# Optimization experiments

Measured on AMD Instinct MI355X. Metric: run time of the kernel, lower is better.

Reference implementation:

```python
import jax, jax.numpy as jnp
import numpy as np

N = 8192
E = 262144
H = 64


def setup_inputs() -> dict:
    key = jax.random.key(0)
    ks = jax.random.split(key, 9)
    edge_index = jax.random.randint(ks[0], (2, E), 0, N, dtype=jnp.int64)
    edge_attr = jax.random.uniform(ks[1], (E,), dtype=jnp.float32)
    node_features = jax.random.normal(ks[2], (N, N), dtype=jnp.float32)
    # GCNConv weights (glorot-ish scale) and biases
    W1 = jax.random.normal(ks[3], (N, H), dtype=jnp.float32) / np.sqrt(N)
    b1 = jnp.zeros((H,), dtype=jnp.float32)
    W2 = jax.random.normal(ks[4], (H, H), dtype=jnp.float32) / np.sqrt(H)
    b2 = jnp.zeros((H,), dtype=jnp.float32)
    fcW = jax.random.normal(ks[5], (H, N), dtype=jnp.float32) / np.sqrt(H)
    fcb = jnp.zeros((N,), dtype=jnp.float32)
    return {"edge_index": edge_index, "edge_attr": edge_attr,
            "node_features": node_features,
            "W1": W1, "b1": b1, "W2": W2, "b2": b2,
            "fcW": fcW, "fcb": fcb}


def _gcn_conv(x, W, b, src, dst, ew, n_nodes):
    # PyG GCNConv with edge weights: x' = D^{-1/2} (A + I) D^{-1/2} (x W) + b
    # src/dst/ew already include self-loops (weight 1.0).
    x = x @ W                                        # [N, out]
    deg = jax.ops.segment_sum(ew, dst, num_segments=n_nodes)  # in-degree w/ loops
    dinv = jax.lax.rsqrt(deg)                        # deg >= 1 due to self loops
    norm = dinv[src] * ew * dinv[dst]                # [E+N]
    out = jax.ops.segment_sum(x[src] * norm[:, None], dst, num_segments=n_nodes)
    return out + b


def reference(edge_index, edge_attr, node_features, W1, b1, W2, b2, fcW, fcb):
    n_nodes = node_features.shape[0]
    loops = jnp.arange(n_nodes, dtype=edge_index.dtype)
    src = jnp.concatenate([edge_index[0], loops])
    dst = jnp.concatenate([edge_index[1], loops])
    ew = jnp.concatenate([edge_attr, jnp.ones((n_nodes,), edge_attr.dtype)])
    x = jax.nn.relu(_gcn_conv(node_features, W1, b1, src, dst, ew, n_nodes))
    x = jax.nn.relu(_gcn_conv(x, W2, b2, src, dst, ew, n_nodes))
    x = x @ fcW + fcb
    return jax.nn.softmax(x, axis=-1)
```

## Files before the change

kernel.cpp:

```cpp
#include <hip/hip_runtime.h>


#define NN 8192
#define NE 262144
#define HD 64
#define KCH 1024
#define NKC 8

typedef float f32x4 __attribute__((ext_vector_type(4)));
typedef short v8s   __attribute__((ext_vector_type(8)));
typedef unsigned short ushort_t;

__device__ __forceinline__ unsigned short bf16_rne(float f){
  union { float f; unsigned u; } v; v.f = f;
  unsigned r = v.u + 0x7fffu + ((v.u >> 16) & 1u);
  return (unsigned short)(r >> 16);
}
__device__ __forceinline__ float bf16_f32(unsigned short h){
  union { unsigned u; float f; } v; v.u = ((unsigned)h) << 16;
  return v.f;
}
__device__ __forceinline__ f32x4 mfma16(v8s a, v8s b, f32x4 c){
  return __builtin_amdgcn_mfma_f32_16x16x32_bf16(a, b, c, 0, 0, 0);
}

__global__ void k_prep0(const float* __restrict__ W1, const float* __restrict__ fcW,
                        ushort_t* w1hi, ushort_t* w1lo, ushort_t* fcwp,
                        float* deg, int* cnt, int* wcnt, float* S){
  int idx = blockIdx.x*blockDim.x + threadIdx.x;
  if (idx < NN){ deg[idx]=1.0f; cnt[idx]=0; wcnt[idx]=0; S[idx]=0.0f; }
  {
    int kk = idx & 31, c = (idx>>5)&15, nt = (idx>>9)&3, kb = idx>>11;
    int k = kb*32 + kk, col = nt*16 + c;
    float w = W1[(size_t)k*HD + col];
    unsigned short hi = bf16_rne(w);
    w1hi[idx] = hi;
    w1lo[idx] = bf16_rne(w - bf16_f32(hi));
  }
  {
    int kk = idx & 31, c = (idx>>5)&15, cblk = (idx>>9)&511, kb = idx>>18;
    int k = kb*32 + kk, col = cblk*16 + c;
    fcwp[idx] = bf16_rne(fcW[(size_t)k*NN + col]);
  }
}

__global__ void k_deg_cnt(const int* ei, const float* ew, float* deg, int* cnt){
  int e = blockIdx.x*blockDim.x + threadIdx.x;
  if (e < NE){
    int d = ei[NE + e];
    atomicAdd(&deg[d], ew[e]);
    atomicAdd(&cnt[d], 1);
  }
}

__global__ void k_scan(const int* cnt, const float* deg, int* rowptr, float* dinv){
  __shared__ int part[256];
  int t = threadIdx.x;
  int loc[32]; int s = 0;
  #pragma unroll
  for (int j=0;j<32;++j){ loc[j] = cnt[t*32+j]; s += loc[j]; }
  part[t] = s; __syncthreads();
  for (int off=1; off<256; off<<=1){
    int v = (t >= off) ? part[t-off] : 0;
    __syncthreads();
    part[t] += v;
    __syncthreads();
  }
  int run = part[t] - s;
  #pragma unroll
  for (int j=0;j<32;++j){ rowptr[t*32+j] = run; run += loc[j]; }
  if (t == 255) rowptr[NN] = run;
  #pragma unroll
  for (int j=0;j<32;++j) dinv[t*32+j] = 1.0f / sqrtf(deg[t*32+j]);
}

__global__ void k_fill(const int* ei, const float* ew, const float* dinv,
                       const int* rowptr, int* wcnt, int* csr_src, float* csr_nrm){
  int e = blockIdx.x*blockDim.x + threadIdx.x;
  if (e < NE){
    int s = ei[e], d = ei[NE+e];
    int slot = rowptr[d] + atomicAdd(&wcnt[d], 1);
    csr_src[slot] = s;
    csr_nrm[slot] = dinv[s] * ew[e] * dinv[d];
  }
}

__global__ __launch_bounds__(256) void k_gemm1(const float* __restrict__ X,
                                               const ushort_t* __restrict__ w1hi,
                                               const ushort_t* __restrict__ w1lo,
                                               float* __restrict__ xw1p){
  int lane = threadIdx.x & 63, w = threadIdx.x >> 6;
  int r = lane & 15, seg = lane >> 4;
  int row = blockIdx.x*64 + w*16 + r;
  int kb0 = blockIdx.y * KCH;
  const float* xr = X + (size_t)row * NN + kb0 + seg*8;

  f32x4 z = {0.f,0.f,0.f,0.f};
  f32x4 acc[4] = {z,z,z,z};

  f32x4 p0 = *(const f32x4*)(xr);
  f32x4 p1 = *(const f32x4*)(xr + 4);

  for (int it = 0; it < KCH/32; ++it){
    f32x4 c0 = p0, c1 = p1;
    if (it < KCH/32 - 1){
      p0 = *(const f32x4*)(xr + (it+1)*32);
      p1 = *(const f32x4*)(xr + (it+1)*32 + 4);
    }
    v8s ah, al;
    #pragma unroll
    for (int j=0;j<4;++j){
      float f = c0[j]; unsigned short h = bf16_rne(f);
      ah[j] = (short)h; al[j] = (short)bf16_rne(f - bf16_f32(h));
      f = c1[j]; h = bf16_rne(f);
      ah[4+j] = (short)h; al[4+j] = (short)bf16_rne(f - bf16_f32(h));
    }
    int kbb = (kb0 >> 5) + it;
    #pragma unroll
    for (int nt=0; nt<4; ++nt){
      size_t boff = ((size_t)(kbb*4 + nt)*16 + r)*32 + seg*8;
      v8s bh = *(const v8s*)(w1hi + boff);
      v8s bl = *(const v8s*)(w1lo + boff);
      acc[nt] = mfma16(ah, bh, acc[nt]);
      acc[nt] = mfma16(ah, bl, acc[nt]);
      acc[nt] = mfma16(al, bh, acc[nt]);
    }
  }

  float* o = xw1p + (size_t)blockIdx.y*(NN*HD) + (size_t)(blockIdx.x*64 + w*16)*HD;
  #pragma unroll
  for (int nt=0; nt<4; ++nt)
    #pragma unroll
    for (int j=0;j<4;++j)
      o[(4*seg + j)*HD + nt*16 + r] = acc[nt][j];
}

__global__ __launch_bounds__(256) void k_red(const float* __restrict__ xw1p,
                                             float* __restrict__ xw1){
  int i = blockIdx.x*blockDim.x + threadIdx.x;
  f32x4 s = {0.f,0.f,0.f,0.f};
  #pragma unroll
  for (int c=0;c<NKC;++c){
    f32x4 v = *(const f32x4*)(xw1p + (size_t)c*NN*HD + (size_t)i*4);
    s[0]+=v[0]; s[1]+=v[1]; s[2]+=v[2]; s[3]+=v[3];
  }
  *(f32x4*)(xw1 + (size_t)i*4) = s;
}

__global__ __launch_bounds__(256) void k_agg1c(const float* __restrict__ xin,
                                               const float* __restrict__ b1,
                                               const float* __restrict__ W2,
                                               const float* __restrict__ dinv,
                                               const int* __restrict__ rowptr,
                                               const int* __restrict__ csr_src,
                                               const float* __restrict__ csr_nrm,
                                               float* __restrict__ x2w){
  __shared__ float W2s[64*64];
  __shared__ float rows[4][64];
  int lane = threadIdx.x & 63, w = threadIdx.x >> 6;
  for (int o = threadIdx.x; o < 64*64; o += 256) W2s[o] = W2[o];
  __syncthreads();

  int i = blockIdx.x*4 + w;
  float di = dinv[i];
  float acc = di*di * xin[(size_t)i*HD + lane];
  int e = rowptr[i], e1 = rowptr[i+1];
  for (; e + 1 < e1; e += 2){
    int s0 = csr_src[e], s1 = csr_src[e+1];
    float n0 = csr_nrm[e], n1 = csr_nrm[e+1];
    acc += n0 * xin[(size_t)s0*HD + lane];
    acc += n1 * xin[(size_t)s1*HD + lane];
  }
  if (e < e1) acc += csr_nrm[e] * xin[(size_t)csr_src[e]*HD + lane];
  float v = acc + b1[lane];
  rows[w][lane] = v > 0.f ? v : 0.f;
  __syncthreads();

  float acc2 = 0.f;
  #pragma unroll
  for (int k=0;k<64;++k) acc2 += rows[w][k] * W2s[k*64 + lane];
  x2w[(size_t)i*HD + lane] = acc2;
}

__global__ __launch_bounds__(256) void k_agg2(const float* __restrict__ xin,
                                              const float* __restrict__ b2,
                                              const float* __restrict__ dinv,
                                              const int* __restrict__ rowptr,
                                              const int* __restrict__ csr_src,
                                              const float* __restrict__ csr_nrm,
                                              ushort_t* __restrict__ x2b){
  int lane = threadIdx.x & 63, w = threadIdx.x >> 6;
  int i = blockIdx.x*4 + w;
  float di = dinv[i];
  float acc = di*di * xin[(size_t)i*HD + lane];
  int e = rowptr[i], e1 = rowptr[i+1];
  for (; e + 1 < e1; e += 2){
    int s0 = csr_src[e], s1 = csr_src[e+1];
    float n0 = csr_nrm[e], n1 = csr_nrm[e+1];
    acc += n0 * xin[(size_t)s0*HD + lane];
    acc += n1 * xin[(size_t)s1*HD + lane];
  }
  if (e < e1) acc += csr_nrm[e] * xin[(size_t)csr_src[e]*HD + lane];
  float v = acc + b2[lane];
  v = v > 0.f ? v : 0.f;
  x2b[(size_t)i*HD + lane] = bf16_rne(v);
}

__global__ __launch_bounds__(256) void k_rowsum(const ushort_t* __restrict__ x2b,
                                                const ushort_t* __restrict__ fcwp,
                                                const float* __restrict__ fcb,
                                                float* __restrict__ S){
  int lane = threadIdx.x & 63, w = threadIdx.x >> 6;
  int r = lane & 15, seg = lane >> 4;
  int row0 = blockIdx.x*128 + w*32;
  const ushort_t* xb = x2b + (size_t)(row0 + r)*HD + seg*8;
  v8s x00 = *(const v8s*)(xb);
  v8s x01 = *(const v8s*)(xb + 32);
  v8s x10 = *(const v8s*)(xb + 16*HD);
  v8s x11 = *(const v8s*)(xb + 16*HD + 32);
  float rp0 = 0.f, rp1 = 0.f;
  for (int cb=0; cb<4; ++cb){
    int colbase = blockIdx.y*256 + cb*64;
    f32x4 z = {0.f,0.f,0.f,0.f};
    f32x4 acc0[4] = {z,z,z,z}, acc1[4] = {z,z,z,z};
    #pragma unroll
    for (int nt=0; nt<4; ++nt){
      int cblk = (colbase >> 4) + nt;
      v8s bA = *(const v8s*)(fcwp + ((size_t)cblk*16 + r)*32 + seg*8);
      v8s bB = *(const v8s*)(fcwp + ((size_t)(512 + cblk)*16 + r)*32 + seg*8);
      acc0[nt] = mfma16(bA, x00, acc0[nt]);
      acc0[nt] = mfma16(bB, x01, acc0[nt]);
      acc1[nt] = mfma16(bA, x10, acc1[nt]);
      acc1[nt] = mfma16(bB, x11, acc1[nt]);
    }
    #pragma unroll
    for (int nt=0; nt<4; ++nt){
      int col = colbase + nt*16 + seg*4;
      f32x4 fb = *(const f32x4*)(fcb + col);
      #pragma unroll
      for (int j=0;j<4;++j){
        rp0 += __expf(acc0[nt][j] + fb[j]);
        rp1 += __expf(acc1[nt][j] + fb[j]);
      }
    }
  }
  rp0 += __shfl_xor(rp0, 16); rp0 += __shfl_xor(rp0, 32);
  rp1 += __shfl_xor(rp1, 16); rp1 += __shfl_xor(rp1, 32);
  if (lane < 16){
    atomicAdd(&S[row0 + lane],      rp0);
    atomicAdd(&S[row0 + 16 + lane], rp1);
  }
}

__global__ __launch_bounds__(256) void k_passB(const ushort_t* __restrict__ x2b,
                                               const ushort_t* __restrict__ fcwp,
                                               const float* __restrict__ fcb,
                                               const float* __restrict__ S,
                                               float* __restrict__ out){
  int lane = threadIdx.x & 63, w = threadIdx.x >> 6;
  int r = lane & 15, seg = lane >> 4;
  int row0 = blockIdx.x*128 + w*32;
  const ushort_t* xb = x2b + (size_t)(row0 + r)*HD + seg*8;
  v8s x00 = *(const v8s*)(xb);
  v8s x01 = *(const v8s*)(xb + 32);
  v8s x10 = *(const v8s*)(xb + 16*HD);
  v8s x11 = *(const v8s*)(xb + 16*HD + 32);
  float si0 = 1.0f / S[row0 + r];
  float si1 = 1.0f / S[row0 + 16 + r];
  float* o0 = out + (size_t)(row0 + r)*NN;
  float* o1 = out + (size_t)(row0 + 16 + r)*NN;
  for (int cb=0; cb<4; ++cb){
    int colbase = blockIdx.y*256 + cb*64;
    f32x4 z = {0.f,0.f,0.f,0.f};
    f32x4 acc0[4] = {z,z,z,z}, acc1[4] = {z,z,z,z};
    #pragma unroll
    for (int nt=0; nt<4; ++nt){
      int cblk = (colbase >> 4) + nt;
      v8s bA = *(const v8s*)(fcwp + ((size_t)cblk*16 + r)*32 + seg*8);
      v8s bB = *(const v8s*)(fcwp + ((size_t)(512 + cblk)*16 + r)*32 + seg*8);
      acc0[nt] = mfma16(bA, x00, acc0[nt]);
      acc0[nt] = mfma16(bB, x01, acc0[nt]);
      acc1[nt] = mfma16(bA, x10, acc1[nt]);
      acc1[nt] = mfma16(bB, x11, acc1[nt]);
    }
    #pragma unroll
    for (int nt=0; nt<4; ++nt){
      int col = colbase + nt*16 + seg*4;
      f32x4 fb = *(const f32x4*)(fcb + col);
      f32x4 v0, v1;
      #pragma unroll
      for (int j=0;j<4;++j){
        v0[j] = __expf(acc0[nt][j] + fb[j]) * si0;
        v1[j] = __expf(acc1[nt][j] + fb[j]) * si1;
      }
      *(f32x4*)(o0 + col) = v0;
      *(f32x4*)(o1 + col) = v1;
    }
  }
}

extern "C" void kernel_launch(void* const* d_in, const int* in_sizes, int n_in,
                              void* d_out, int out_size, void* d_ws, size_t ws_size,
                              hipStream_t stream){
  (void)in_sizes; (void)n_in; (void)out_size; (void)ws_size;
  const int*   ei  = (const int*)  d_in[0];
  const float* ew  = (const float*)d_in[1];
  const float* X   = (const float*)d_in[2];
  const float* W1  = (const float*)d_in[3];
  const float* b1  = (const float*)d_in[4];
  const float* W2  = (const float*)d_in[5];
  const float* b2  = (const float*)d_in[6];
  const float* fcW = (const float*)d_in[7];
  const float* fcb = (const float*)d_in[8];
  float* out = (float*)d_out;
  char*  ws  = (char*)d_ws;

  float*    deg     = (float*)   (ws + 0);
  float*    dinv    = (float*)   (ws + 32768);
  int*      cnt     = (int*)     (ws + 65536);
  int*      wcnt    = (int*)     (ws + 98304);
  int*      rowptr  = (int*)     (ws + 131072);
  int*      csr_src = (int*)     (ws + 167936);
  float*    csr_nrm = (float*)   (ws + 1216512);
  ushort_t* w1hi    = (ushort_t*)(ws + 2265088);
  ushort_t* w1lo    = (ushort_t*)(ws + 3313664);
  ushort_t* fcwp    = (ushort_t*)(ws + 4362240);
  float*    xw1p    = (float*)   (ws + 5410816);
  float*    xw1     = (float*)   (ws + 22188032);
  float*    x2w     = (float*)   (ws + 24285184);
  ushort_t* x2b     = (ushort_t*)(ws + 26382336);
  float*    S       = (float*)   (ws + 27430912);

  k_prep0   <<<2048, 256, 0, stream>>>(W1, fcW, w1hi, w1lo, fcwp, deg, cnt, wcnt, S);
  k_deg_cnt <<<1024, 256, 0, stream>>>(ei, ew, deg, cnt);
  k_scan    <<<1,    256, 0, stream>>>(cnt, deg, rowptr, dinv);
  k_fill    <<<1024, 256, 0, stream>>>(ei, ew, dinv, rowptr, wcnt, csr_src, csr_nrm);
  k_gemm1   <<<dim3(128, NKC), 256, 0, stream>>>(X, w1hi, w1lo, xw1p);
  k_red     <<<512,  256, 0, stream>>>(xw1p, xw1);
  k_agg1c   <<<2048, 256, 0, stream>>>(xw1, b1, W2, dinv, rowptr, csr_src, csr_nrm, x2w);
  k_agg2    <<<2048, 256, 0, stream>>>(x2w, b2, dinv, rowptr, csr_src, csr_nrm, x2b);
  k_rowsum  <<<dim3(64,32), 256, 0, stream>>>(x2b, fcwp, fcb, S);
  k_passB   <<<dim3(64,32), 256, 0, stream>>>(x2b, fcwp, fcb, S, out);
}
```

Baseline: 320.8 us.

## Cast X to bf16 once and stage gemm1 tiles through swizzled LDS

Adds a pre-pass that converts the 8192x8192 fp32 feature matrix to bf16 in the output buffer. The first GEMM then reads bf16 tiles into double-buffered, XOR-swizzled shared memory using direct global-to-LDS loads. The split-bf16 hi/lo three-MFMA scheme becomes a single bf16 MFMA, cutting matrix work and per-thread conversion. In exchange it adds a full extra read and write pass over X and loses precision in the first layer's product.

```diff
diff --git a/kernel.cpp b/kernel.cpp
--- a/kernel.cpp
+++ b/kernel.cpp
@@ -6,6 +6,7 @@
 #define HD 64
 #define KCH 1024
 #define NKC 8
+#define NTS (KCH/64)
 
 typedef float f32x4 __attribute__((ext_vector_type(4)));
 typedef short v8s   __attribute__((ext_vector_type(8)));
@@ -23,9 +24,28 @@
 __device__ __forceinline__ f32x4 mfma16(v8s a, v8s b, f32x4 c){
   return __builtin_amdgcn_mfma_f32_16x16x32_bf16(a, b, c, 0, 0, 0);
 }
+__device__ __forceinline__ void gload16(const void* g, void* l){
+  __builtin_amdgcn_global_load_lds(
+      (const __attribute__((address_space(1))) unsigned int*)g,
+      (__attribute__((address_space(3))) unsigned int*)l, 16, 0, 0);
+}
+
+__global__ __launch_bounds__(256) void k_xcast(const float* __restrict__ X,
+                                               ushort_t* __restrict__ xb){
+  size_t i = ((size_t)blockIdx.x*256 + threadIdx.x)*8;
+  f32x4 a = *(const f32x4*)(X + i);
+  f32x4 b = *(const f32x4*)(X + i + 4);
+  v8s o;
+  #pragma unroll
+  for (int j=0;j<4;++j){
+    o[j]   = (short)bf16_rne(a[j]);
+    o[4+j] = (short)bf16_rne(b[j]);
+  }
+  *(v8s*)(xb + i) = o;
+}
 
 __global__ void k_prep0(const float* __restrict__ W1, const float* __restrict__ fcW,
-                        ushort_t* w1hi, ushort_t* w1lo, ushort_t* fcwp,
+                        ushort_t* w1hi, ushort_t* fcwp,
                         float* deg, int* cnt, int* wcnt, float* S){
   int idx = blockIdx.x*blockDim.x + threadIdx.x;
   if (idx < NN){ deg[idx]=1.0f; cnt[idx]=0; wcnt[idx]=0; S[idx]=0.0f; }
@@ -33,9 +53,9 @@
     int kk = idx & 31, c = (idx>>5)&15, nt = (idx>>9)&3, kb = idx>>11;
     int k = kb*32 + kk, col = nt*16 + c;
     float w = W1[(size_t)k*HD + col];
-    unsigned short hi = bf16_rne(w);
-    w1hi[idx] = hi;
-    w1lo[idx] = bf16_rne(w - bf16_f32(hi));
+    int chunk = idx >> 3, e = idx & 7;
+    int sidx = ((chunk ^ (c & 7)) << 3) | e;
+    w1hi[sidx] = bf16_rne(w);
   }
   {
     int kk = idx & 31, c = (idx>>5)&15, cblk = (idx>>9)&511, kb = idx>>18;
@@ -85,49 +105,72 @@
   }
 }
 
-__global__ __launch_bounds__(256) void k_gemm1(const float* __restrict__ X,
-                                               const ushort_t* __restrict__ w1hi,
-                                               const ushort_t* __restrict__ w1lo,
-                                               float* __restrict__ xw1p){
+__global__ __launch_bounds__(256, 4) void k_gemm1(const ushort_t* __restrict__ Xb,
+                                                  const ushort_t* __restrict__ w1hi,
+                                                  float* __restrict__ xw1p){
+  __shared__ __align__(16) char sA[2][8192];
+  __shared__ __align__(16) char sB[2][8192];
   int lane = threadIdx.x & 63, w = threadIdx.x >> 6;
   int r = lane & 15, seg = lane >> 4;
-  int row = blockIdx.x*64 + w*16 + r;
-  int kb0 = blockIdx.y * KCH;
-  const float* xr = X + (size_t)row * NN + kb0 + seg*8;
+  int c8 = lane & 7, r8 = lane >> 3;
+  int row0 = blockIdx.x*64, kb0 = blockIdx.y*KCH;
+
+  const char* Xc  = (const char*)Xb;
+  const char* w1c = (const char*)w1hi;
+  size_t asrc[2];
+  #pragma unroll
+  for (int i=0;i<2;++i){
+    int rl = w*16 + i*8 + r8;
+    asrc[i] = (size_t)(row0 + rl)*(NN*2) + (size_t)kb0*2 + (size_t)((c8 ^ r8)*16);
+  }
+
+  int aoff[2];
+  #pragma unroll
+  for (int ks=0; ks<2; ++ks)
+    aoff[ks] = (w*16 + r)*128 + (((ks*4 + seg) ^ (r & 7)) << 4);
+  int bc[4];
+  #pragma unroll
+  for (int nt=0; nt<4; ++nt)
+    bc[nt] = ((nt*64 + r*4 + seg) ^ (r & 7)) << 4;
 
   f32x4 z = {0.f,0.f,0.f,0.f};
   f32x4 acc[4] = {z,z,z,z};
 
-  f32x4 p0 = *(const f32x4*)(xr);
-  f32x4 p1 = *(const f32x4*)(xr + 4);
-
-  for (int it = 0; it < KCH/32; ++it){
-    f32x4 c0 = p0, c1 = p1;
-    if (it < KCH/32 - 1){
-      p0 = *(const f32x4*)(xr + (it+1)*32);
-      p1 = *(const f32x4*)(xr + (it+1)*32 + 4);
-    }
-    v8s ah, al;
-    #pragma unroll
-    for (int j=0;j<4;++j){
-      float f = c0[j]; unsigned short h = bf16_rne(f);
-      ah[j] = (short)h; al[j] = (short)bf16_rne(f - bf16_f32(h));
-      f = c1[j]; h = bf16_rne(f);
-      ah[4+j] = (short)h; al[4+j] = (short)bf16_rne(f - bf16_f32(h));
-    }
-    int kbb = (kb0 >> 5) + it;
-    #pragma unroll
-    for (int nt=0; nt<4; ++nt){
-      size_t boff = ((size_t)(kbb*4 + nt)*16 + r)*32 + seg*8;
-      v8s bh = *(const v8s*)(w1hi + boff);
-      v8s bl = *(const v8s*)(w1lo + boff);
-      acc[nt] = mfma16(ah, bh, acc[nt]);
-      acc[nt] = mfma16(ah, bl, acc[nt]);
-      acc[nt] = mfma16(al, bh, acc[nt]);
-    }
-  }
-
-  float* o = xw1p + (size_t)blockIdx.y*(NN*HD) + (size_t)(blockIdx.x*64 + w*16)*HD;
+  auto STAGE = [&](int t, int b){
+    char* aD = (char*)sA[b] + w*2048;
+    gload16(Xc + asrc[0] + (size_t)t*128, aD);
+    gload16(Xc + asrc[1] + (size_t)t*128, aD + 1024);
+    size_t sBo = ((size_t)(kb0 >> 5) + 2*t)*4096 + w*1024 + lane*16;
+    gload16(w1c + sBo,        (char*)sB[b] + w*1024);
+    gload16(w1c + sBo + 4096, (char*)sB[b] + 4096 + w*1024);
+  };
+
+  STAGE(0, 0);
+
+  for (int t = 0; t < NTS; ++t){
+    int cur = t & 1;
+    if (t + 1 < NTS){
+      STAGE(t+1, cur^1);
+      asm volatile("s_waitcnt vmcnt(4)" ::: "memory");
+    } else {
+      asm volatile("s_waitcnt vmcnt(0)" ::: "memory");
+    }
+    __builtin_amdgcn_s_barrier();
+    __builtin_amdgcn_sched_barrier(0);
+    #pragma unroll
+    for (int ks=0; ks<2; ++ks){
+      v8s a = *(const v8s*)(&sA[cur][aoff[ks]]);
+      #pragma unroll
+      for (int nt=0; nt<4; ++nt){
+        v8s b = *(const v8s*)(&sB[cur][ks*4096 + bc[nt]]);
+        acc[nt] = mfma16(a, b, acc[nt]);
+      }
+    }
+    __builtin_amdgcn_sched_barrier(0);
+    __builtin_amdgcn_s_barrier();
+  }
+
+  float* o = xw1p + (size_t)blockIdx.y*(NN*HD) + (size_t)(row0 + w*16)*HD;
   #pragma unroll
   for (int nt=0; nt<4; ++nt)
     #pragma unroll
@@ -323,7 +366,6 @@
   int*      csr_src = (int*)     (ws + 167936);
   float*    csr_nrm = (float*)   (ws + 1216512);
   ushort_t* w1hi    = (ushort_t*)(ws + 2265088);
-  ushort_t* w1lo    = (ushort_t*)(ws + 3313664);
   ushort_t* fcwp    = (ushort_t*)(ws + 4362240);
   float*    xw1p    = (float*)   (ws + 5410816);
   float*    xw1     = (float*)   (ws + 22188032);
@@ -331,14 +373,17 @@
   ushort_t* x2b     = (ushort_t*)(ws + 26382336);
   float*    S       = (float*)   (ws + 27430912);
 
-  k_prep0   <<<2048, 256, 0, stream>>>(W1, fcW, w1hi, w1lo, fcwp, deg, cnt, wcnt, S);
-  k_deg_cnt <<<1024, 256, 0, stream>>>(ei, ew, deg, cnt);
-  k_scan    <<<1,    256, 0, stream>>>(cnt, deg, rowptr, dinv);
-  k_fill    <<<1024, 256, 0, stream>>>(ei, ew, dinv, rowptr, wcnt, csr_src, csr_nrm);
-  k_gemm1   <<<dim3(128, NKC), 256, 0, stream>>>(X, w1hi, w1lo, xw1p);
-  k_red     <<<512,  256, 0, stream>>>(xw1p, xw1);
-  k_agg1c   <<<2048, 256, 0, stream>>>(xw1, b1, W2, dinv, rowptr, csr_src, csr_nrm, x2w);
-  k_agg2    <<<2048, 256, 0, stream>>>(x2w, b2, dinv, rowptr, csr_src, csr_nrm, x2b);
+  ushort_t* Xbf = (ushort_t*)d_out;
+
+  k_prep0   <<<2048,  256, 0, stream>>>(W1, fcW, w1hi, fcwp, deg, cnt, wcnt, S);
+  k_xcast   <<<32768, 256, 0, stream>>>(X, Xbf);
+  k_deg_cnt <<<1024,  256, 0, stream>>>(ei, ew, deg, cnt);
+  k_scan    <<<1,     256, 0, stream>>>(cnt, deg, rowptr, dinv);
+  k_fill    <<<1024,  256, 0, stream>>>(ei, ew, dinv, rowptr, wcnt, csr_src, csr_nrm);
+  k_gemm1   <<<dim3(128, NKC), 256, 0, stream>>>(Xbf, w1hi, xw1p);
+  k_red     <<<512,   256, 0, stream>>>(xw1p, xw1);
+  k_agg1c   <<<2048,  256, 0, stream>>>(xw1, b1, W2, dinv, rowptr, csr_src, csr_nrm, x2w);
+  k_agg2    <<<2048,  256, 0, stream>>>(x2w, b2, dinv, rowptr, csr_src, csr_nrm, x2b);
   k_rowsum  <<<dim3(64,32), 256, 0, stream>>>(x2b, fcwp, fcb, S);
   k_passB   <<<dim3(64,32), 256, 0, stream>>>(x2b, fcwp, fcb, S, out);
 }
```

After: 296.0 us. 7.7% less time.

## Drop split-bf16 correction terms in GEMM1 and deepen load prefetching

Applied to the files above, without the earlier changes.

The first GEMM (X @ W1) now uses a single bf16 MFMA per tile instead of three hi/lo split-precision MFMAs, so the low-part W1 buffer and its preparation are removed. The K loop is fully unrolled, with a 4-deep register prefetch ring for X and a 2-deep ring for W1 fragments, and launch bounds ask for 4 blocks per CU. The aim is to cut MFMA count and conversion ALU work in a GEMM that reads the full 256MB X matrix, and to overlap its memory latency better. In exchange, GEMM1 accuracy drops to plain bf16 products over a K of 8192, which may approach the tolerance, and the larger prefetch buffers raise register pressure.

```diff
diff --git a/kernel.cpp b/kernel.cpp
--- a/kernel.cpp
+++ b/kernel.cpp
@@ -25,17 +25,14 @@
 }
 
 __global__ void k_prep0(const float* __restrict__ W1, const float* __restrict__ fcW,
-                        ushort_t* w1hi, ushort_t* w1lo, ushort_t* fcwp,
+                        ushort_t* w1hi, ushort_t* fcwp,
                         float* deg, int* cnt, int* wcnt, float* S){
   int idx = blockIdx.x*blockDim.x + threadIdx.x;
   if (idx < NN){ deg[idx]=1.0f; cnt[idx]=0; wcnt[idx]=0; S[idx]=0.0f; }
   {
     int kk = idx & 31, c = (idx>>5)&15, nt = (idx>>9)&3, kb = idx>>11;
     int k = kb*32 + kk, col = nt*16 + c;
-    float w = W1[(size_t)k*HD + col];
-    unsigned short hi = bf16_rne(w);
-    w1hi[idx] = hi;
-    w1lo[idx] = bf16_rne(w - bf16_f32(hi));
+    w1hi[idx] = bf16_rne(W1[(size_t)k*HD + col]);
   }
   {
     int kk = idx & 31, c = (idx>>5)&15, cblk = (idx>>9)&511, kb = idx>>18;
@@ -85,49 +82,60 @@
   }
 }
 
-__global__ __launch_bounds__(256) void k_gemm1(const float* __restrict__ X,
-                                               const ushort_t* __restrict__ w1hi,
-                                               const ushort_t* __restrict__ w1lo,
-                                               float* __restrict__ xw1p){
+__global__ __launch_bounds__(256, 4) void k_gemm1(const float* __restrict__ X,
+                                                  const ushort_t* __restrict__ w1hi,
+                                                  float* __restrict__ xw1p){
   int lane = threadIdx.x & 63, w = threadIdx.x >> 6;
   int r = lane & 15, seg = lane >> 4;
-  int row = blockIdx.x*64 + w*16 + r;
+  int row0 = blockIdx.x*64 + w*16;
   int kb0 = blockIdx.y * KCH;
-  const float* xr = X + (size_t)row * NN + kb0 + seg*8;
+  const float* xr = X + (size_t)(row0 + r)*NN + kb0 + seg*8;
+  const ushort_t* bp = w1hi + ((size_t)(kb0 >> 5))*2048 + r*32 + seg*8;
 
   f32x4 z = {0.f,0.f,0.f,0.f};
   f32x4 acc[4] = {z,z,z,z};
 
-  f32x4 p0 = *(const f32x4*)(xr);
-  f32x4 p1 = *(const f32x4*)(xr + 4);
-
-  for (int it = 0; it < KCH/32; ++it){
-    f32x4 c0 = p0, c1 = p1;
-    if (it < KCH/32 - 1){
-      p0 = *(const f32x4*)(xr + (it+1)*32);
-      p1 = *(const f32x4*)(xr + (it+1)*32 + 4);
-    }
-    v8s ah, al;
+  f32x4 pa[4][2];
+  v8s   pb[2][4];
+
+  #pragma unroll
+  for (int p=0;p<4;++p){
+    pa[p][0] = *(const f32x4*)(xr + p*32);
+    pa[p][1] = *(const f32x4*)(xr + p*32 + 4);
+  }
+  #pragma unroll
+  for (int p=0;p<2;++p)
+    #pragma unroll
+    for (int nt=0;nt<4;++nt)
+      pb[p][nt] = *(const v8s*)(bp + (size_t)p*2048 + nt*512);
+
+  #pragma unroll
+  for (int t=0; t<32; ++t){
+    const int sa = t & 3, sb = t & 1;
+    f32x4 a0 = pa[sa][0], a1 = pa[sa][1];
+    v8s b0 = pb[sb][0], b1 = pb[sb][1], b2 = pb[sb][2], b3 = pb[sb][3];
+    if (t + 4 < 32){
+      pa[sa][0] = *(const f32x4*)(xr + (t+4)*32);
+      pa[sa][1] = *(const f32x4*)(xr + (t+4)*32 + 4);
+    }
+    if (t + 2 < 32){
+      #pragma unroll
+      for (int nt=0;nt<4;++nt)
+        pb[sb][nt] = *(const v8s*)(bp + (size_t)(t+2)*2048 + nt*512);
+    }
+    v8s ah;
     #pragma unroll
     for (int j=0;j<4;++j){
-      float f = c0[j]; unsigned short h = bf16_rne(f);
-      ah[j] = (short)h; al[j] = (short)bf16_rne(f - bf16_f32(h));
-      f = c1[j]; h = bf16_rne(f);
-      ah[4+j] = (short)h; al[4+j] = (short)bf16_rne(f - bf16_f32(h));
-    }
-    int kbb = (kb0 >> 5) + it;
-    #pragma unroll
-    for (int nt=0; nt<4; ++nt){
-      size_t boff = ((size_t)(kbb*4 + nt)*16 + r)*32 + seg*8;
-      v8s bh = *(const v8s*)(w1hi + boff);
-      v8s bl = *(const v8s*)(w1lo + boff);
-      acc[nt] = mfma16(ah, bh, acc[nt]);
-      acc[nt] = mfma16(ah, bl, acc[nt]);
-      acc[nt] = mfma16(al, bh, acc[nt]);
-    }
-  }
-
-  float* o = xw1p + (size_t)blockIdx.y*(NN*HD) + (size_t)(blockIdx.x*64 + w*16)*HD;
+      ah[j]   = (short)bf16_rne(a0[j]);
+      ah[4+j] = (short)bf16_rne(a1[j]);
+    }
+    acc[0] = mfma16(ah, b0, acc[0]);
+    acc[1] = mfma16(ah, b1, acc[1]);
+    acc[2] = mfma16(ah, b2, acc[2]);
+    acc[3] = mfma16(ah, b3, acc[3]);
+  }
+
+  float* o = xw1p + (size_t)blockIdx.y*(NN*HD) + (size_t)row0*HD;
   #pragma unroll
   for (int nt=0; nt<4; ++nt)
     #pragma unroll
@@ -323,7 +331,6 @@
   int*      csr_src = (int*)     (ws + 167936);
   float*    csr_nrm = (float*)   (ws + 1216512);
   ushort_t* w1hi    = (ushort_t*)(ws + 2265088);
-  ushort_t* w1lo    = (ushort_t*)(ws + 3313664);
   ushort_t* fcwp    = (ushort_t*)(ws + 4362240);
   float*    xw1p    = (float*)   (ws + 5410816);
   float*    xw1     = (float*)   (ws + 22188032);
@@ -331,11 +338,11 @@
   ushort_t* x2b     = (ushort_t*)(ws + 26382336);
   float*    S       = (float*)   (ws + 27430912);
 
-  k_prep0   <<<2048, 256, 0, stream>>>(W1, fcW, w1hi, w1lo, fcwp, deg, cnt, wcnt, S);
+  k_prep0   <<<2048, 256, 0, stream>>>(W1, fcW, w1hi, fcwp, deg, cnt, wcnt, S);
   k_deg_cnt <<<1024, 256, 0, stream>>>(ei, ew, deg, cnt);
   k_scan    <<<1,    256, 0, stream>>>(cnt, deg, rowptr, dinv);
   k_fill    <<<1024, 256, 0, stream>>>(ei, ew, dinv, rowptr, wcnt, csr_src, csr_nrm);
-  k_gemm1   <<<dim3(128, NKC), 256, 0, stream>>>(X, w1hi, w1lo, xw1p);
+  k_gemm1   <<<dim3(128, NKC), 256, 0, stream>>>(X, w1hi, xw1p);
   k_red     <<<512,  256, 0, stream>>>(xw1p, xw1);
   k_agg1c   <<<2048, 256, 0, stream>>>(xw1, b1, W2, dinv, rowptr, csr_src, csr_nrm, x2w);
   k_agg2    <<<2048, 256, 0, stream>>>(x2w, b2, dinv, rowptr, csr_src, csr_nrm, x2b);
```

Result: faster. 308.3 us (-3.9%).
